# Performance work log

Hardware: AMD Instinct MI355X
Metric: run time of the kernel (lower is better)

## Reference

```python
import jax, jax.numpy as jnp
import numpy as np

N = 16384      # tokens
D_IN = 256     # input feature dim
D = 1024       # d_model
H = 2048       # expert hidden dim (2 * d_model)
E = 8          # n_experts
K = 2          # top_k
OUT = 2        # output classes
EPS = 1e-5


def layernorm(x, g, b):
    m = jnp.mean(x, axis=-1, keepdims=True)
    v = jnp.mean(jnp.square(x - m), axis=-1, keepdims=True)
    return (x - m) * jax.lax.rsqrt(v + EPS) * g + b


def setup_inputs() -> dict:
    key = jax.random.key(0)
    ks = jax.random.split(key, 10)
    s_in = 1.0 / np.sqrt(D_IN)
    s_d = 1.0 / np.sqrt(D)
    s_h = 1.0 / np.sqrt(H)
    return {
        "x": jax.random.normal(ks[0], (N, D_IN), jnp.float32),
        "w_in": jax.random.normal(ks[1], (D_IN, D), jnp.float32) * s_in,
        "b_in": jnp.zeros((D,), jnp.float32),
        "g_in": jnp.ones((D,), jnp.float32),
        "beta_in": jnp.zeros((D,), jnp.float32),
        "w_gate": jax.random.normal(ks[2], (D, E), jnp.float32) * s_d,
        "w1": jax.random.normal(ks[3], (E, D, H), jnp.float32) * s_d,
        "b1": jnp.zeros((E, H), jnp.float32),
        "w2": jax.random.normal(ks[4], (E, H, D), jnp.float32) * s_h,
        "b2": jnp.zeros((E, D), jnp.float32),
        "g_moe": jnp.ones((D,), jnp.float32),
        "beta_moe": jnp.zeros((D,), jnp.float32),
        "g_out": jnp.ones((D,), jnp.float32),
        "beta_out": jnp.zeros((D,), jnp.float32),
        "w_cls": jax.random.normal(ks[5], (D, OUT), jnp.float32) * s_d,
        "b_cls": jnp.zeros((OUT,), jnp.float32),
    }


def reference(x, w_in, b_in, g_in, beta_in, w_gate, w1, b1, w2, b2,
              g_moe, beta_moe, g_out, beta_out, w_cls, b_cls):
    # input projection + norm
    h = layernorm(x @ w_in + b_in, g_in, beta_in)            # [N, D]
    # router: softmax then top-k, renormalize over selected experts
    probs = jax.nn.softmax(h @ w_gate, axis=-1)              # [N, E]
    _, top_idx = jax.lax.top_k(probs, K)                     # [N, K]
    sel = jax.nn.one_hot(top_idx, E, dtype=probs.dtype).sum(axis=1)  # [N, E] 0/1
    gates = probs * sel
    gates = gates / (jnp.sum(gates, axis=-1, keepdims=True) + 1e-9)
    # experts: weighted combine; gate==0 tokens contribute nothing (same math
    # as the torch masked gather/scatter-add, dropout off in eval)
    mixed = jnp.zeros_like(h)
    for e in range(E):  # fixed, small expert count
        expert_out = jax.nn.gelu(h @ w1[e] + b1[e]) @ w2[e] + b2[e]  # [N, D]
        mixed = mixed + gates[:, e:e + 1] * expert_out
    out = layernorm(h + mixed, g_moe, beta_moe)
    out = layernorm(out, g_out, beta_out)
    return out @ w_cls + b_cls                               # [N, OUT]
```

## Files before the change

### kernel.cpp

```cpp
#include <hip/hip_runtime.h>
#include <hip/hip_bf16.h>

#define D_IN 256
#define DM   1024
#define HD   2048
#define NE   8
#define NTOK 16384

typedef __attribute__((ext_vector_type(8))) short short8;
typedef __attribute__((ext_vector_type(4))) float f32x4;
typedef unsigned int uint;

#define MT_TOFF1 0
#define MT_TOFF2 512
#define MT_CNT1  1536
#define MT_P1    1600
#define MT_OFF1  1664
#define MT_CNT2  1728
#define MT_PCNT2 1856
#define MT_TOTAL 1984

__device__ inline ushort f2bf(float v){
  __hip_bfloat16 b = __float2bfloat16(v);
  return *reinterpret_cast<ushort*>(&b);
}
__device__ inline float bf2f(ushort u){
  __hip_bfloat16 b = *reinterpret_cast<__hip_bfloat16*>(&u);
  return __bfloat162float(b);
}

__device__ inline float gelu_fast(float x){
  float u = 0.7978845608028654f * x * (1.0f + 0.044715f*x*x);
  return x / (1.0f + __expf(-2.0f*u));
}

__device__ inline void gload16(const void* g, void* l){
  __builtin_amdgcn_global_load_lds(
      (const __attribute__((address_space(1))) void*)g,
      (__attribute__((address_space(3))) void*)l, 16, 0, 0);
}


__global__ __launch_bounds__(256) void transpose_bf16_kernel(
    const float* __restrict__ src, ushort* __restrict__ dst, int R, int C)
{
  __shared__ float tile[32][33];
  int e = blockIdx.z;
  src += (size_t)e*R*C; dst += (size_t)e*R*C;
  int c0 = blockIdx.x*32, r0 = blockIdx.y*32;
  int tx = threadIdx.x & 31, ty = threadIdx.x >> 5;
  #pragma unroll
  for (int rr = ty; rr < 32; rr += 8)
    tile[rr][tx] = src[(size_t)(r0+rr)*C + c0+tx];
  __syncthreads();
  #pragma unroll
  for (int rr = ty; rr < 32; rr += 8)
    dst[(size_t)(c0+rr)*R + r0+tx] = f2bf(tile[tx][rr]);
}

__global__ __launch_bounds__(256) void split_x_kernel(
    const float* __restrict__ x, ushort* __restrict__ xs3)
{
  int g = blockIdx.x*256 + threadIdx.x;
  int e0 = g*4;
  int row = e0 >> 8, col = e0 & 255;
  f32x4 v = *(const f32x4*)(x + (size_t)row*D_IN + col);
  ushort4 hi, mi, lo;
  #pragma unroll
  for (int i=0;i<4;++i){
    float f = v[i];
    ushort h = f2bf(f);       float fh = bf2f(h);
    ushort m = f2bf(f - fh);  float fm = bf2f(m);
    ushort l = f2bf(f - fh - fm);
    ((ushort*)&hi)[i]=h; ((ushort*)&mi)[i]=m; ((ushort*)&lo)[i]=l;
  }
  ushort* base = xs3 + (size_t)row*768 + col;
  *(ushort4*)(base)       = hi;
  *(ushort4*)(base + 256) = mi;
  *(ushort4*)(base + 512) = lo;
}

__global__ __launch_bounds__(256) void transpose_split3_kernel(
    const float* __restrict__ src, ushort* __restrict__ dst)
{
  __shared__ float tile[32][33];
  int c0 = blockIdx.x*32, r0 = blockIdx.y*32;
  int tx = threadIdx.x & 31, ty = threadIdx.x >> 5;
  #pragma unroll
  for (int rr = ty; rr < 32; rr += 8)
    tile[rr][tx] = src[(size_t)(r0+rr)*DM + c0+tx];
  __syncthreads();
  #pragma unroll
  for (int rr = ty; rr < 32; rr += 8){
    float f = tile[tx][rr];
    ushort h = f2bf(f);       float fh = bf2f(h);
    ushort m = f2bf(f - fh);  float fm = bf2f(m);
    ushort l = f2bf(f - fh - fm);
    ushort* d = dst + (size_t)(c0+rr)*768 + r0 + tx;
    d[0]   = h;
    d[256] = m;
    d[512] = l;
  }
}

__global__ __launch_bounds__(256) void wgate_t_kernel(
    const float* __restrict__ w_gate, float* __restrict__ wgt)
{
  int e = blockIdx.x;
  for (int j = threadIdx.x; j < DM; j += 256)
    wgt[(size_t)e*DM + j] = w_gate[(size_t)j*NE + e];
}

__global__ __launch_bounds__(256) void gemm_router(
    const ushort* __restrict__ A,
    const ushort* __restrict__ BT,
    const float* __restrict__ b_in,
    float* __restrict__ y)
{
  __shared__ ushort As[3][128*32];
  __shared__ ushort Bs[3][128*32];
  const int tid = threadIdx.x;
  const int w = tid>>6, l = tid&63;
  const int wm = w>>1, wn = w&1;
  const int bm0 = blockIdx.y*128, bn0 = blockIdx.x*128;
  const int lr = l&15, lk = l>>4;
  const int rsub = l>>2;
  const int csub = ((l&3) ^ ((l>>3)&3)) * 8;

  const ushort* ag[2]; const ushort* bg[2];
  int aslot[2];
  #pragma unroll
  for (int i=0;i<2;++i){
    int ra = bm0 + w*32 + i*16 + rsub;
    int rb = bn0 + w*32 + i*16 + rsub;
    ag[i] = A  + (size_t)ra*768 + csub;
    bg[i] = BT + (size_t)rb*768 + csub;
    aslot[i] = (w*32 + i*16)*32;
  }

  const int pOffT[6] = {0,256,0,256,512,0};
  const int qOffT[6] = {0,0,256,256,0,512};
  auto stage = [&](int db, int t){
    int pOff = pOffT[t>>3] + (t&7)*32;
    int qOff = qOffT[t>>3] + (t&7)*32;
    #pragma unroll
    for (int i=0;i<2;++i){
      gload16(ag[i]+pOff, (ushort*)As[db] + aslot[i]);
      gload16(bg[i]+qOff, (ushort*)Bs[db] + aslot[i]);
    }
  };

  f32x4 acc[4][4] = {};
  const int NK = 48;
  stage(0, 0); stage(1, 1);
  int cur = 0;
  for (int t=0; t<NK; ++t){
    int sb = cur - 1; if (sb < 0) sb = 2;
    if (t+2 < NK)     { stage(sb, t+2); asm volatile("s_waitcnt vmcnt(8)" ::: "memory"); }
    else if (t+1 < NK){                 asm volatile("s_waitcnt vmcnt(4)" ::: "memory"); }
    else              {                 asm volatile("s_waitcnt vmcnt(0)" ::: "memory"); }
    __builtin_amdgcn_s_barrier();
    short8 af[4], bf[4];
    #pragma unroll
    for (int i=0;i<4;++i)
      af[i] = *(const short8*)(As[cur] + (wm*64 + i*16 + lr)*32 + (lk ^ ((lr>>1)&3))*8);
    #pragma unroll
    for (int j=0;j<4;++j)
      bf[j] = *(const short8*)(Bs[cur] + (wn*64 + j*16 + lr)*32 + (lk ^ ((lr>>1)&3))*8);
    #pragma unroll
    for (int i=0;i<4;++i){
      #pragma unroll
      for (int j=0;j<4;++j)
        acc[i][j] = __builtin_amdgcn_mfma_f32_16x16x32_bf16(af[i], bf[j], acc[i][j], 0, 0, 0);
    }
    __builtin_amdgcn_s_barrier();
    cur = cur + 1; if (cur > 2) cur = 0;
  }

  #pragma unroll
  for (int i=0;i<4;++i){
    #pragma unroll
    for (int j=0;j<4;++j){
      int n = bn0 + wn*64 + j*16 + lr;
      float bn_ = b_in[n];
      #pragma unroll
      for (int r=0;r<4;++r){
        int m = bm0 + wm*64 + i*16 + lk*4 + r;
        y[(size_t)m*DM + n] = acc[i][j][r] + bn_;
      }
    }
  }
}

__device__ inline double wredd(double v){
  #pragma unroll
  for (int o=32;o>0;o>>=1) v += __shfl_xor(v, o, 64);
  return v;
}

__global__ __launch_bounds__(256) void ln_router_kernel(
    const float* __restrict__ g_in, const float* __restrict__ beta_in,
    const float* __restrict__ wgt,
    ushort* __restrict__ hbf, float* __restrict__ resid,
    float* __restrict__ gates, int* __restrict__ selmask)
{
  int tok = blockIdx.x*4 + (threadIdx.x>>6);
  int l = threadIdx.x & 63;
  float* row = resid + (size_t)tok*DM;
  float u[16];
  double s=0.0, q=0.0;
  #pragma unroll
  for (int r=0;r<16;++r){ u[r]=row[l+64*r]; s+=u[r]; q+=(double)u[r]*u[r]; }
  s = wredd(s); q = wredd(q);
  double mean = s*(1.0/1024.0);
  double var  = q*(1.0/1024.0) - mean*mean;
  double rstd = 1.0/sqrt(var + 1e-5);

  double lg[NE];
  #pragma unroll
  for (int e=0;e<NE;++e) lg[e]=0.0;
  float hv[16];
  #pragma unroll
  for (int r=0;r<16;++r){
    int j = l + 64*r;
    double v = ((double)u[r]-mean)*rstd*(double)g_in[j] + (double)beta_in[j];
    hv[r] = (float)v;
    #pragma unroll
    for (int e=0;e<NE;++e) lg[e] += v*(double)wgt[(size_t)e*DM + j];
  }
  #pragma unroll
  for (int r=0;r<16;++r){
    int j = l + 64*r;
    row[j] = hv[r];
    hbf[(size_t)tok*DM + j] = f2bf(hv[r]);
  }
  #pragma unroll
  for (int e=0;e<NE;++e) lg[e] = wredd(lg[e]);

  if (l==0){
    double mx = lg[0];
    #pragma unroll
    for (int e=1;e<NE;++e) mx = lg[e]>mx ? lg[e] : mx;
    double p[NE]; double sum=0.0;
    #pragma unroll
    for (int e=0;e<NE;++e){ p[e]=exp(lg[e]-mx); sum+=p[e]; }
    #pragma unroll
    for (int e=0;e<NE;++e) p[e]/=sum;
    int i1=0;
    for (int e=1;e<NE;++e) if (p[e]>p[i1]) i1=e;
    int i2=-1;
    for (int e=0;e<NE;++e){ if (e==i1) continue; if (i2<0 || p[e]>p[i2]) i2=e; }
    double denom = p[i1]+p[i2]+1e-9;
    float g[NE];
    #pragma unroll
    for (int e=0;e<NE;++e) g[e]=0.f;
    g[i1]=(float)(p[i1]/denom);
    g[i2]=(float)(p[i2]/denom);
    #pragma unroll
    for (int e=0;e<NE;++e) gates[(size_t)tok*NE+e]=g[e];
    selmask[tok] = (1<<i1)|(1<<i2);
  }
}

__global__ __launch_bounds__(256) void builder_count(
    const int* __restrict__ selmask, uint* __restrict__ bc1, uint* __restrict__ bc2)
{
  __shared__ uint c1[8], c2s[16];
  int b = blockIdx.x, tid = threadIdx.x;
  if (tid<8) c1[tid]=0;
  if (tid<16) c2s[tid]=0;
  __syncthreads();
  int m = selmask[b*256+tid];
  int ea = __ffs(m)-1, eb = 31-__clz(m);
  atomicAdd(&c1[ea],1u); atomicAdd(&c1[eb],1u);
  atomicAdd(&c2s[ea],1u); atomicAdd(&c2s[8+eb],1u);
  __syncthreads();
  if (tid<8) bc1[b*8+tid]=c1[tid];
  if (tid<16) bc2[b*16+tid]=c2s[tid];
}

__global__ __launch_bounds__(256) void builder_scan(
    const uint* __restrict__ bc1, const uint* __restrict__ bc2,
    uint* __restrict__ meta, int nch, int TPC)
{
  int tid = threadIdx.x;
  int c = tid/24, k = tid%24;
  if (c < nch){
    if (k < 8){
      uint run=0;
      for (int b=c*TPC; b<(c+1)*TPC; ++b){ meta[MT_TOFF1 + b*8 + k] = run; run += bc1[b*8+k]; }
      meta[MT_CNT1 + c*8 + k] = run;
    } else {
      int k2 = k-8;
      uint run=0;
      for (int b=c*TPC; b<(c+1)*TPC; ++b){ meta[MT_TOFF2 + b*16 + k2] = run; run += bc2[b*16+k2]; }
      meta[MT_CNT2 + c*16 + k2] = run;
      meta[MT_PCNT2 + c*16 + k2] = ((run + 127u)/128u)*128u;
    }
  }
  __syncthreads();
  if (tid < nch){
    uint off=0;
    for (int e=0;e<8;++e){
      uint cn = meta[MT_CNT1 + tid*8 + e];
      uint p = ((cn+127u)/128u)*128u;
      meta[MT_P1 + tid*8 + e] = p;
      meta[MT_OFF1 + tid*8 + e] = off;
      off += p;
    }
  }
}

__device__ inline int exclscan256(int v, int* sc, int tid){
  sc[tid]=v; __syncthreads();
  #pragma unroll
  for (int o=1;o<256;o<<=1){
    int x = (tid>=o) ? sc[tid-o] : 0;
    __syncthreads();
    sc[tid]+=x;
    __syncthreads();
  }
  int incl = sc[tid]; __syncthreads();
  return incl - v;
}

__global__ __launch_bounds__(256) void builder_fill(
    const int* __restrict__ selmask, const uint* __restrict__ meta,
    int* __restrict__ ids1, int CH)
{
  __shared__ int sc[256];
  int b = blockIdx.x, tid = threadIdx.x;
  int t = b*256 + tid;
  int c = t / CH;
  int m = selmask[t];
  int ea = __ffs(m)-1, eb = 31-__clz(m);
  int ja=0, jb=0;
  for (int e=0;e<8;++e){
    int r0 = exclscan256((ea==e)?1:0, sc, tid);
    if (ea==e) ja = r0;
    int r1 = exclscan256((eb==e)?1:0, sc, tid);
    if (eb==e) jb = r1;
  }
  {
    uint j    = meta[MT_TOFF2 + b*16 + ea] + (uint)ja;
    ids1[(c*8+ea)*CH + j] = t;
  }
  {
    uint j    = meta[MT_TOFF2 + b*16 + 8 + eb] + (uint)jb;
    uint pos1 = meta[MT_CNT2 + c*16 + eb] + j;
    ids1[(c*8+eb)*CH + pos1] = t;
  }
}

__global__ __launch_bounds__(256) void gemm_ffn1(
    const ushort* __restrict__ Abase,
    const ushort* __restrict__ BT,
    const int*   __restrict__ rows,
    const uint*  __restrict__ pcnt,
    const uint*  __restrict__ off1,
    const float* __restrict__ bias,
    ushort* __restrict__ t1,
    int K, int N, int CH)
{
  const int e = blockIdx.z;
  const int bm0 = blockIdx.y*128;
  if ((uint)bm0 >= pcnt[e]) return;
  const int bn0 = blockIdx.x*128;

  __shared__ ushort As[3][128*32];
  __shared__ ushort Bs[3][128*32];
  const int tid = threadIdx.x;
  const int w = tid>>6, l = tid&63;
  const int wm = w>>1, wn = w&1;
  const int lr = l&15, lk = l>>4;
  const int rsub = l>>2;
  const int csub = ((l&3) ^ ((l>>3)&3)) * 8;

  const ushort* ag[2]; const ushort* bg[2];
  int slot[2];
  #pragma unroll
  for (int i=0;i<2;++i){
    int ra = w*32 + i*16 + rsub;
    int id = rows[e*CH + bm0 + ra];
    ag[i] = Abase + (size_t)id*K + csub;
    int rb = bn0 + w*32 + i*16 + rsub;
    bg[i] = BT + (size_t)e*N*K + (size_t)rb*K + csub;
    slot[i] = (w*32 + i*16)*32;
  }

  auto stage = [&](int db, int kt){
    #pragma unroll
    for (int i=0;i<2;++i){
      gload16(ag[i]+kt, (ushort*)As[db] + slot[i]);
      gload16(bg[i]+kt, (ushort*)Bs[db] + slot[i]);
    }
  };

  f32x4 acc[4][4] = {};
  const int NK = K>>5;
  stage(0, 0); stage(1, 32);
  int cur = 0;
  for (int t=0; t<NK; ++t){
    int sb = cur - 1; if (sb < 0) sb = 2;
    if (t+2 < NK)     { stage(sb, (t+2)<<5); asm volatile("s_waitcnt vmcnt(8)" ::: "memory"); }
    else if (t+1 < NK){                      asm volatile("s_waitcnt vmcnt(4)" ::: "memory"); }
    else              {                      asm volatile("s_waitcnt vmcnt(0)" ::: "memory"); }
    __builtin_amdgcn_s_barrier();
    short8 af[4], bf[4];
    #pragma unroll
    for (int i=0;i<4;++i)
      af[i] = *(const short8*)(As[cur] + (wm*64 + i*16 + lr)*32 + (lk ^ ((lr>>1)&3))*8);
    #pragma unroll
    for (int j=0;j<4;++j)
      bf[j] = *(const short8*)(Bs[cur] + (wn*64 + j*16 + lr)*32 + (lk ^ ((lr>>1)&3))*8);
    #pragma unroll
    for (int i=0;i<4;++i){
      #pragma unroll
      for (int j=0;j<4;++j)
        acc[i][j] = __builtin_amdgcn_mfma_f32_16x16x32_bf16(af[i], bf[j], acc[i][j], 0, 0, 0);
    }
    __builtin_amdgcn_s_barrier();
    cur = cur + 1; if (cur > 2) cur = 0;
  }

  #pragma unroll
  for (int i=0;i<4;++i){
    #pragma unroll
    for (int j=0;j<4;++j){
      int n = bn0 + wn*64 + j*16 + lr;
      float bn_ = bias[(size_t)e*N + n];
      #pragma unroll
      for (int r=0;r<4;++r){
        int mloc = wm*64 + i*16 + lk*4 + r;
        float v = acc[i][j][r] + bn_;
        size_t trow = (size_t)off1[e] + bm0 + mloc;
        t1[trow*N + n] = f2bf(gelu_fast(v));
      }
    }
  }
}

template<int SLOT>
__global__ __launch_bounds__(256) void gemm_ffn2(
    const ushort* __restrict__ t1,
    const ushort* __restrict__ BT,
    const int*   __restrict__ ids1,
    const uint*  __restrict__ cnt2,
    const uint*  __restrict__ pcnt2,
    const uint*  __restrict__ off1,
    const float* __restrict__ bias,
    const float* __restrict__ gates,
    float* __restrict__ resid,
    int K, int N, int CH)
{
  const int e = blockIdx.z;
  const int bm0 = blockIdx.y*128;
  if ((uint)bm0 >= pcnt2[SLOT*8 + e]) return;
  const uint scnt  = cnt2[SLOT*8 + e];
  const uint start = (SLOT==1) ? cnt2[e] : 0u;
  const int bn0 = blockIdx.x*128;

  __shared__ ushort As[3][128*32];
  __shared__ ushort Bs[3][128*32];
  const int tid = threadIdx.x;
  const int w = tid>>6, l = tid&63;
  const int wm = w>>1, wn = w&1;
  const int lr = l&15, lk = l>>4;
  const int rsub = l>>2;
  const int csub = ((l&3) ^ ((l>>3)&3)) * 8;

  const ushort* ag[2]; const ushort* bg[2];
  int slot[2];
  #pragma unroll
  for (int i=0;i<2;++i){
    int ra = w*32 + i*16 + rsub;
    size_t arow = (size_t)off1[e] + start + bm0 + ra;
    ag[i] = t1 + arow*K + csub;
    int rb = bn0 + w*32 + i*16 + rsub;
    bg[i] = BT + (size_t)e*N*K + (size_t)rb*K + csub;
    slot[i] = (w*32 + i*16)*32;
  }

  auto stage = [&](int db, int kt){
    #pragma unroll
    for (int i=0;i<2;++i){
      gload16(ag[i]+kt, (ushort*)As[db] + slot[i]);
      gload16(bg[i]+kt, (ushort*)Bs[db] + slot[i]);
    }
  };

  f32x4 acc[4][4] = {};
  const int NK = K>>5;
  stage(0, 0); stage(1, 32);
  int cur = 0;
  for (int t=0; t<NK; ++t){
    int sb = cur - 1; if (sb < 0) sb = 2;
    if (t+2 < NK)     { stage(sb, (t+2)<<5); asm volatile("s_waitcnt vmcnt(8)" ::: "memory"); }
    else if (t+1 < NK){                      asm volatile("s_waitcnt vmcnt(4)" ::: "memory"); }
    else              {                      asm volatile("s_waitcnt vmcnt(0)" ::: "memory"); }
    __builtin_amdgcn_s_barrier();
    short8 af[4], bf[4];
    #pragma unroll
    for (int i=0;i<4;++i)
      af[i] = *(const short8*)(As[cur] + (wm*64 + i*16 + lr)*32 + (lk ^ ((lr>>1)&3))*8);
    #pragma unroll
    for (int j=0;j<4;++j)
      bf[j] = *(const short8*)(Bs[cur] + (wn*64 + j*16 + lr)*32 + (lk ^ ((lr>>1)&3))*8);
    #pragma unroll
    for (int i=0;i<4;++i){
      #pragma unroll
      for (int j=0;j<4;++j)
        acc[i][j] = __builtin_amdgcn_mfma_f32_16x16x32_bf16(af[i], bf[j], acc[i][j], 0, 0, 0);
    }
    __builtin_amdgcn_s_barrier();
    cur = cur + 1; if (cur > 2) cur = 0;
  }

  #pragma unroll
  for (int i=0;i<4;++i){
    #pragma unroll
    for (int j=0;j<4;++j){
      int n = bn0 + wn*64 + j*16 + lr;
      float bn_ = bias[(size_t)e*N + n];
      #pragma unroll
      for (int r=0;r<4;++r){
        int mloc = wm*64 + i*16 + lk*4 + r;
        int mg = bm0 + mloc;
        if ((uint)mg < scnt){
          int tok = ids1[e*CH + (int)start + mg];
          float g = gates[(size_t)tok*NE + e];
          resid[(size_t)tok*N + n] += g*(acc[i][j][r] + bn_);
        }
      }
    }
  }
}

__global__ __launch_bounds__(256) void final_kernel(
    const float* __restrict__ resid,
    const float* __restrict__ g_moe, const float* __restrict__ beta_moe,
    const float* __restrict__ g_out, const float* __restrict__ beta_out,
    const float* __restrict__ w_cls, const float* __restrict__ b_cls,
    float* __restrict__ out)
{
  int tok = blockIdx.x*4 + (threadIdx.x>>6);
  int l = threadIdx.x & 63;
  const float* row = resid + (size_t)tok*DM;
  float u[16];
  double s=0.0,q=0.0;
  #pragma unroll
  for (int r=0;r<16;++r){ u[r]=row[l + 64*r]; s+=u[r]; q+=(double)u[r]*u[r]; }
  s=wredd(s); q=wredd(q);
  double m1 = s*(1.0/1024.0), v1 = q*(1.0/1024.0)-m1*m1;
  double rs1 = 1.0/sqrt(v1+1e-5);
  float tv[16]; double s2=0.0,q2=0.0;
  #pragma unroll
  for (int r=0;r<16;++r){
    int j = l+64*r;
    float vv = (float)((u[r]-m1)*rs1)*g_moe[j] + beta_moe[j];
    tv[r]=vv; s2+=vv; q2+=(double)vv*vv;
  }
  s2=wredd(s2); q2=wredd(q2);
  double m2=s2*(1.0/1024.0), v2=q2*(1.0/1024.0)-m2*m2;
  double rs2=1.0/sqrt(v2+1e-5);
  double p0=0.0,p1=0.0;
  #pragma unroll
  for (int r=0;r<16;++r){
    int j=l+64*r;
    double y=((double)tv[r]-m2)*rs2*(double)g_out[j]+(double)beta_out[j];
    p0+=y*(double)w_cls[j*2]; p1+=y*(double)w_cls[j*2+1];
  }
  p0=wredd(p0); p1=wredd(p1);
  if (l==0){
    out[(size_t)tok*2  ]=(float)(p0+(double)b_cls[0]);
    out[(size_t)tok*2+1]=(float)(p1+(double)b_cls[1]);
  }
}

extern "C" void kernel_launch(void* const* d_in, const int* in_sizes, int n_in,
                              void* d_out, int out_size, void* d_ws, size_t ws_size,
                              hipStream_t stream)
{
  (void)in_sizes; (void)n_in; (void)out_size;
  const float* x       = (const float*)d_in[0];
  const float* w_in    = (const float*)d_in[1];
  const float* b_in    = (const float*)d_in[2];
  const float* g_in    = (const float*)d_in[3];
  const float* beta_in = (const float*)d_in[4];
  const float* w_gate  = (const float*)d_in[5];
  const float* w1      = (const float*)d_in[6];
  const float* b1      = (const float*)d_in[7];
  const float* w2      = (const float*)d_in[8];
  const float* b2      = (const float*)d_in[9];
  const float* g_moe   = (const float*)d_in[10];
  const float* beta_mo = (const float*)d_in[11];
  const float* g_out   = (const float*)d_in[12];
  const float* beta_ou = (const float*)d_in[13];
  const float* w_cls   = (const float*)d_in[14];
  const float* b_cls   = (const float*)d_in[15];
  float* out = (float*)d_out;

  char* p = (char*)d_ws;
  ushort* w1t   = (ushort*)p; p += (size_t)NE*HD*DM*2;
  ushort* w2t   = (ushort*)p; p += (size_t)NE*DM*HD*2;
  ushort* hbf   = (ushort*)p; p += (size_t)NTOK*DM*2;
  float*  resid = (float*)p;  p += (size_t)NTOK*DM*4;
  float*  gates = (float*)p;  p += (size_t)NTOK*NE*4;
  int*    selmk = (int*)p;    p += (size_t)NTOK*4;
  int*    ids1  = (int*)p;    p += (size_t)NE*NTOK*4;
  ushort* wt3   = (ushort*)p; p += (size_t)DM*768*2;
  float*  wgt   = (float*)p;  p += (size_t)NE*DM*4;
  uint*   bc1   = (uint*)p;   p += (size_t)64*8*4;
  uint*   bc2   = (uint*)p;   p += (size_t)64*16*4;
  uint*   meta  = (uint*)p;   p += (size_t)MT_TOTAL*4;
  size_t fixed = (size_t)(p - (char*)d_ws);

  const size_t xs3_bytes = (size_t)NTOK*768*2;
  size_t t1b1 = ((size_t)2*NTOK        + 2048)*HD*2;
  size_t t1b2 = ((size_t)2*(NTOK/2)    + 2048)*HD*2;
  size_t t1b4 = ((size_t)2*(NTOK/4)    + 2048)*HD*2;
  int nch = 8;
  if      (ws_size >= fixed + (t1b1 > xs3_bytes ? t1b1 : xs3_bytes)) nch = 1;
  else if (ws_size >= fixed + (t1b2 > xs3_bytes ? t1b2 : xs3_bytes)) nch = 2;
  else if (ws_size >= fixed + (t1b4 > xs3_bytes ? t1b4 : xs3_bytes)) nch = 4;
  const int CH  = NTOK/nch;
  const int TPC = CH/256;
  ushort* t1  = (ushort*)p;
  ushort* xs3 = (ushort*)p;

  split_x_kernel<<<dim3(NTOK*D_IN/4/256), 256, 0, stream>>>(x, xs3);
  transpose_split3_kernel<<<dim3(DM/32, D_IN/32), 256, 0, stream>>>(w_in, wt3);
  wgate_t_kernel<<<dim3(NE), 256, 0, stream>>>(w_gate, wgt);
  transpose_bf16_kernel<<<dim3(HD/32, DM/32, NE), 256, 0, stream>>>(w1, w1t, DM, HD);
  transpose_bf16_kernel<<<dim3(DM/32, HD/32, NE), 256, 0, stream>>>(w2, w2t, HD, DM);

  gemm_router<<<dim3(DM/128, NTOK/128), 256, 0, stream>>>(xs3, wt3, b_in, resid);
  ln_router_kernel<<<dim3(NTOK/4), 256, 0, stream>>>(g_in, beta_in, wgt,
                                                     hbf, resid, gates, selmk);

  hipMemsetAsync(ids1, 0, (size_t)NE*NTOK*4, stream);

  builder_count<<<dim3(NTOK/256), 256, 0, stream>>>(selmk, bc1, bc2);
  builder_scan<<<dim3(1), 256, 0, stream>>>(bc1, bc2, meta, nch, TPC);
  builder_fill<<<dim3(NTOK/256), 256, 0, stream>>>(selmk, meta, ids1, CH);

  for (int c = 0; c < nch; ++c) {
    gemm_ffn1<<<dim3(HD/128, CH/128, NE), 256, 0, stream>>>(
        hbf, w1t, ids1 + (size_t)c*8*CH,
        meta+MT_P1+c*8, meta+MT_OFF1+c*8, b1, t1, DM, HD, CH);
    gemm_ffn2<0><<<dim3(DM/128, CH/128, NE), 256, 0, stream>>>(
        t1, w2t, ids1 + (size_t)c*8*CH,
        meta+MT_CNT2+c*16, meta+MT_PCNT2+c*16, meta+MT_OFF1+c*8,
        b2, gates, resid, HD, DM, CH);
    gemm_ffn2<1><<<dim3(DM/128, CH/128, NE), 256, 0, stream>>>(
        t1, w2t, ids1 + (size_t)c*8*CH,
        meta+MT_CNT2+c*16, meta+MT_PCNT2+c*16, meta+MT_OFF1+c*8,
        b2, gates, resid, HD, DM, CH);
  }

  final_kernel<<<dim3(NTOK/4), 256, 0, stream>>>(resid, g_moe, beta_mo, g_out, beta_ou,
                                                 w_cls, b_cls, out);
}
```

Measured before the change: 892.0 us.

## Merge FFN2 slot launches with atomics, fuse weight transposes, raise MFMA priority

```diff
diff --git a/kernel.cpp b/kernel.cpp
--- a/kernel.cpp
+++ b/kernel.cpp
@@ -41,13 +41,21 @@
 }
 
 
-__global__ __launch_bounds__(256) void transpose_bf16_kernel(
-    const float* __restrict__ src, ushort* __restrict__ dst, int R, int C)
+__global__ __launch_bounds__(256) void transpose_both_kernel(
+    const float* __restrict__ w1, const float* __restrict__ w2,
+    ushort* __restrict__ w1t, ushort* __restrict__ w2t)
 {
   __shared__ float tile[32][33];
-  int e = blockIdx.z;
+  int bid = blockIdx.x;
+  int which = bid >> 14;
+  int r = bid & 16383;
+  const float* src; ushort* dst; int R, C;
+  if (which==0){ src=w1; dst=w1t; R=DM; C=HD; }
+  else         { src=w2; dst=w2t; R=HD; C=DM; }
+  int nbx = C/32, nby = R/32;
+  int e = r / (nbx*nby); int rem = r % (nbx*nby);
+  int c0 = (rem % nbx)*32, r0 = (rem / nbx)*32;
   src += (size_t)e*R*C; dst += (size_t)e*R*C;
-  int c0 = blockIdx.x*32, r0 = blockIdx.y*32;
   int tx = threadIdx.x & 31, ty = threadIdx.x >> 5;
   #pragma unroll
   for (int rr = ty; rr < 32; rr += 8)
@@ -167,12 +175,14 @@
     #pragma unroll
     for (int j=0;j<4;++j)
       bf[j] = *(const short8*)(Bs[cur] + (wn*64 + j*16 + lr)*32 + (lk ^ ((lr>>1)&3))*8);
+    __builtin_amdgcn_s_setprio(1);
     #pragma unroll
     for (int i=0;i<4;++i){
       #pragma unroll
       for (int j=0;j<4;++j)
         acc[i][j] = __builtin_amdgcn_mfma_f32_16x16x32_bf16(af[i], bf[j], acc[i][j], 0, 0, 0);
     }
+    __builtin_amdgcn_s_setprio(0);
     __builtin_amdgcn_s_barrier();
     cur = cur + 1; if (cur > 2) cur = 0;
   }
@@ -413,12 +423,14 @@
     #pragma unroll
     for (int j=0;j<4;++j)
       bf[j] = *(const short8*)(Bs[cur] + (wn*64 + j*16 + lr)*32 + (lk ^ ((lr>>1)&3))*8);
+    __builtin_amdgcn_s_setprio(1);
     #pragma unroll
     for (int i=0;i<4;++i){
       #pragma unroll
       for (int j=0;j<4;++j)
         acc[i][j] = __builtin_amdgcn_mfma_f32_16x16x32_bf16(af[i], bf[j], acc[i][j], 0, 0, 0);
     }
+    __builtin_amdgcn_s_setprio(0);
     __builtin_amdgcn_s_barrier();
     cur = cur + 1; if (cur > 2) cur = 0;
   }
@@ -440,7 +452,6 @@
   }
 }
 
-template<int SLOT>
 __global__ __launch_bounds__(256) void gemm_ffn2(
     const ushort* __restrict__ t1,
     const ushort* __restrict__ BT,
@@ -453,11 +464,12 @@
     float* __restrict__ resid,
     int K, int N, int CH)
 {
-  const int e = blockIdx.z;
+  const int z = blockIdx.z;
+  const int e = z & 7, sl = z >> 3;
   const int bm0 = blockIdx.y*128;
-  if ((uint)bm0 >= pcnt2[SLOT*8 + e]) return;
-  const uint scnt  = cnt2[SLOT*8 + e];
-  const uint start = (SLOT==1) ? cnt2[e] : 0u;
+  if ((uint)bm0 >= pcnt2[sl*8 + e]) return;
+  const uint scnt  = cnt2[sl*8 + e];
+  const uint start = sl ? cnt2[e] : 0u;
   const int bn0 = blockIdx.x*128;
 
   __shared__ ushort As[3][128*32];
@@ -506,12 +518,14 @@
     #pragma unroll
     for (int j=0;j<4;++j)
       bf[j] = *(const short8*)(Bs[cur] + (wn*64 + j*16 + lr)*32 + (lk ^ ((lr>>1)&3))*8);
+    __builtin_amdgcn_s_setprio(1);
     #pragma unroll
     for (int i=0;i<4;++i){
       #pragma unroll
       for (int j=0;j<4;++j)
         acc[i][j] = __builtin_amdgcn_mfma_f32_16x16x32_bf16(af[i], bf[j], acc[i][j], 0, 0, 0);
     }
+    __builtin_amdgcn_s_setprio(0);
     __builtin_amdgcn_s_barrier();
     cur = cur + 1; if (cur > 2) cur = 0;
   }
@@ -529,7 +543,7 @@
         if ((uint)mg < scnt){
           int tok = ids1[e*CH + (int)start + mg];
           float g = gates[(size_t)tok*NE + e];
-          resid[(size_t)tok*N + n] += g*(acc[i][j][r] + bn_);
+          atomicAdd(&resid[(size_t)tok*N + n], g*(acc[i][j][r] + bn_));
         }
       }
     }
@@ -631,8 +645,7 @@
   split_x_kernel<<<dim3(NTOK*D_IN/4/256), 256, 0, stream>>>(x, xs3);
   transpose_split3_kernel<<<dim3(DM/32, D_IN/32), 256, 0, stream>>>(w_in, wt3);
   wgate_t_kernel<<<dim3(NE), 256, 0, stream>>>(w_gate, wgt);
-  transpose_bf16_kernel<<<dim3(HD/32, DM/32, NE), 256, 0, stream>>>(w1, w1t, DM, HD);
-  transpose_bf16_kernel<<<dim3(DM/32, HD/32, NE), 256, 0, stream>>>(w2, w2t, HD, DM);
+  transpose_both_kernel<<<dim3(32768), 256, 0, stream>>>(w1, w2, w1t, w2t);
 
   gemm_router<<<dim3(DM/128, NTOK/128), 256, 0, stream>>>(xs3, wt3, b_in, resid);
   ln_router_kernel<<<dim3(NTOK/4), 256, 0, stream>>>(g_in, beta_in, wgt,
@@ -648,14 +661,10 @@
     gemm_ffn1<<<dim3(HD/128, CH/128, NE), 256, 0, stream>>>(
         hbf, w1t, ids1 + (size_t)c*8*CH,
         meta+MT_P1+c*8, meta+MT_OFF1+c*8, b1, t1, DM, HD, CH);
-    gemm_ffn2<0><<<dim3(DM/128, CH/128, NE), 256, 0, stream>>>(
+    gemm_ffn2<<<dim3(DM/128, CH/128, 2*NE), 256, 0, stream>>>(
         t1, w2t, ids1 + (size_t)c*8*CH,
         meta+MT_CNT2+c*16, meta+MT_PCNT2+c*16, meta+MT_OFF1+c*8,
         b2, gates, resid, HD, DM, CH);
-    gemm_ffn2<1><<<dim3(DM/128, CH/128, NE), 256, 0, stream>>>(
-        t1, w2t, ids1 + (size_t)c*8*CH,
-        meta+MT_CNT2+c*16, meta+MT_PCNT2+c*16, meta+MT_OFF1+c*8,
-        b2, gates, resid, HD, DM, CH);
   }
 
   final_kernel<<<dim3(NTOK/4), 256, 0, stream>>>(resid, g_moe, beta_mo, g_out, beta_ou,
```

Measured after the change: 892.8 us. Within noise of the previous version (+0.1%).
